# Kernel tuning notes

Measured on AMD Instinct MI355X. Metric: run time of the kernel, lower is better.

The kernel has to match this reference:

```python
import jax, jax.numpy as jnp
import numpy as np
import math

PHI = (1.0 + math.sqrt(5.0)) / 2.0
BASE_FAST = PHI
BASE_SLOW = 1618.0
D = 1024
NH = 16
HD = D // NH
H_GATE = max(8, D // 4)
B, L = 2, 2048


def _rope_cos_sin(seq_len, dim, base):
    # dim assumed even here (D=1024)
    idx = jnp.arange(0, dim, 2, dtype=jnp.float32) / float(dim)
    inv = 1.0 / (base ** idx)
    t = jnp.arange(seq_len, dtype=jnp.float32)
    freqs = jnp.outer(t, inv)                      # (L, dim/2)
    emb = jnp.concatenate([freqs, freqs], axis=-1) # (L, dim)
    return jnp.cos(emb), jnp.sin(emb)


def _rotate_half(x):
    d = x.shape[-1]
    x1, x2 = x[..., : d // 2], x[..., d // 2 :]
    return jnp.concatenate([-x2, x1], axis=-1)


def setup_inputs() -> dict:
    key = jax.random.key(0)
    ks = jax.random.split(key, 16)
    std = 0.02
    inp = {
        "z": jax.random.normal(ks[0], (B, L, D), jnp.float32),
        "pool_seq": jax.random.normal(ks[1], (B, L, D), jnp.float32),
        "Wq": std * jax.random.normal(ks[2], (D, D), jnp.float32),
        "bq": jnp.zeros((D,), jnp.float32),
        "Wk": std * jax.random.normal(ks[3], (D, D), jnp.float32),
        "bk": jnp.zeros((D,), jnp.float32),
        "Wv": std * jax.random.normal(ks[4], (D, D), jnp.float32),
        "bv": jnp.zeros((D,), jnp.float32),
        "W_coh": std * jax.random.normal(ks[5], (D, D), jnp.float32),
        "gamma": jnp.zeros((1,), jnp.float32) + 0.1,  # nonzero so bias path is exercised
        "Wg1": std * jax.random.normal(ks[6], (H_GATE, D), jnp.float32),
        "bg1": jnp.zeros((H_GATE,), jnp.float32),
        "Wg2": std * jax.random.normal(ks[7], (1, H_GATE), jnp.float32),
        "bg2": jnp.zeros((1,), jnp.float32),
    }
    return inp


def reference(z, pool_seq, Wq, bq, Wk, bk, Wv, bv, W_coh, gamma, Wg1, bg1, Wg2, bg2):
    b, l, d = z.shape
    # QKV projections (torch Linear: x @ W^T + b)
    Q = z @ Wq.T + bq
    K_raw = z @ Wk.T + bk
    V = z @ Wv.T + bv

    # Global coherence bias: per-query pool vector dotted with every key
    gk = pool_seq @ W_coh.T                                   # (B,L,D)
    gb = jnp.einsum("bqd,bkd->bqk", gk, K_raw) * (d ** -0.5)  # (B,L,L)
    gb = jnp.tanh(gamma[0]) * gb

    # Per-position RoPE interpolation gate (exact GELU as in torch default)
    h = jax.nn.gelu(pool_seq @ Wg1.T + bg1, approximate=False)
    gate = jax.nn.sigmoid(h @ Wg2.T + bg2)                    # (B,L,1)

    cos_f, sin_f = _rope_cos_sin(l, d, BASE_FAST)             # (L,D)
    cos_s, sin_s = _rope_cos_sin(l, d, BASE_SLOW)
    cos = gate * cos_f + (1.0 - gate) * cos_s                 # (B,L,D)
    sin = gate * sin_f + (1.0 - gate) * sin_s

    Q = Q * cos + _rotate_half(Q) * sin
    K_rot = K_raw * cos + _rotate_half(K_raw) * sin

    nh, hd = NH, d // NH
    Q_h = Q.reshape(b, l, nh, hd).transpose(0, 2, 1, 3)       # (B,H,L,hd)
    K_h = K_rot.reshape(b, l, nh, hd).transpose(0, 2, 1, 3)
    V_h = V.reshape(b, l, nh, hd).transpose(0, 2, 1, 3)

    logits = jnp.einsum("bhqd,bhkd->bhqk", Q_h, K_h) * (hd ** -0.5)
    logits = logits + gb[:, None]                             # broadcast over heads

    causal = jnp.tril(jnp.ones((l, l), dtype=bool))
    logits = jnp.where(causal[None, None], logits, -jnp.inf)

    attn_w_h = jax.nn.softmax(logits, axis=-1)                # (B,H,L,L)
    out_h = jnp.einsum("bhqk,bhkd->bhqd", attn_w_h, V_h)
    out = out_h.transpose(0, 2, 1, 3).reshape(b, l, d)
    attn_w = attn_w_h.mean(axis=1)                            # (B,L,L)
    return out, attn_w
```

## Files before the change

### kernel.cpp

```cpp
#include <hip/hip_runtime.h>
#include <hip/hip_bf16.h>

constexpr int Bn  = 2;
constexpr int Ln  = 2048;
constexpr int Dn  = 1024;
constexpr int NH  = 16;
constexpr int HGn = 256;
constexpr long BLD = (long)Bn * Ln * Dn;

typedef float f32x4 __attribute__((ext_vector_type(4)));
typedef float f32x2 __attribute__((ext_vector_type(2)));
typedef short s16x8 __attribute__((ext_vector_type(8)));
typedef short s16x4 __attribute__((ext_vector_type(4)));
typedef short s16x2 __attribute__((ext_vector_type(2)));

#define DEVI static __device__ __forceinline__

DEVI float bf2f(short u) {
  union { float f; unsigned int i; } v; v.i = ((unsigned int)(unsigned short)u) << 16; return v.f;
}
DEVI short f2bf(float f) {
  union { float f; unsigned int i; } v; v.f = f;
  unsigned int r = v.i + 0x7FFFu + ((v.i >> 16) & 1u);
  return (short)(r >> 16);
}
DEVI void gl_lds16(const void* g, void* l) {
  __builtin_amdgcn_global_load_lds((const __attribute__((address_space(1))) unsigned int*)g,
                                   (__attribute__((address_space(3))) unsigned int*)l, 16, 0, 0);
}

struct CastDesc { const float* src[7]; long cum[8]; };
__global__ void k_cast7(CastDesc d, short* __restrict__ dst) {
  long gi = ((long)blockIdx.x * 256 + threadIdx.x) * 4;
  int s = 0;
#pragma unroll
  for (int i = 1; i < 7; ++i) if (gi >= d.cum[i]) s = i;
  const float* sp = d.src[s] + (gi - d.cum[s]);
  f32x4 v = *(const f32x4*)sp;
  s16x4 o; o[0] = f2bf(v[0]); o[1] = f2bf(v[1]); o[2] = f2bf(v[2]); o[3] = f2bf(v[3]);
  *(s16x4*)(dst + gi) = o;
}

__global__ __launch_bounds__(512, 8)
void k_gemm_mega(const short* __restrict__ zb, const short* __restrict__ pb,
                 const short* __restrict__ Wcat,
                 const float* __restrict__ bq, const float* __restrict__ bk,
                 const float* __restrict__ bv, const float* __restrict__ bg1,
                 short* __restrict__ Qp, short* __restrict__ Kp,
                 short* __restrict__ Vtb, short* __restrict__ Gk,
                 short* __restrict__ Hfb) {
  int wgid = blockIdx.x;
  int xcd = wgid & 7, idx = wgid >> 3;
  int n0 = (idx >> 2) * 64;
  int m0 = (xcd * 4 + (idx & 3)) * 128;
  const short* Ap = (n0 < 3072) ? zb : pb;
  __shared__ short smA[2][128 * 32];
  __shared__ short smB[2][64 * 32];
  int tid = threadIdx.x;
  int lane = tid & 63, wid = tid >> 6;
  int wr = wid >> 1, wc = wid & 1;
  int lr = lane & 15, lg = lane >> 4;
  int r_in = lane >> 2;
  int slot = (lane & 3) * 8;
  int scol = ((lane & 3) ^ ((lane >> 3) & 3)) * 8;
  int rsw = (lr >> 1) & 3;
  f32x4 acc[2][2] = {};
  auto stage = [&](int buf, int k0) {
    int rowA = wid * 16 + r_in;
    gl_lds16(Ap + (long)(m0 + rowA) * Dn + k0 + scol, &smA[buf][rowA * 32 + slot]);
    if (wid < 4) {
      int rowB = wid * 16 + r_in;
      gl_lds16(Wcat + (long)(n0 + rowB) * Dn + k0 + scol, &smB[buf][rowB * 32 + slot]);
    }
  };
  stage(0, 0);
  int cur = 0;
  for (int k0 = 0; k0 < Dn; k0 += 32) {
    bool pre = (k0 + 32 < Dn);
    if (pre) stage(cur ^ 1, k0 + 32);
    __builtin_amdgcn_sched_barrier(0);
    if (pre) {
      if (wid < 4) asm volatile("s_waitcnt vmcnt(2)" ::: "memory");
      else         asm volatile("s_waitcnt vmcnt(1)" ::: "memory");
    } else {
      asm volatile("s_waitcnt vmcnt(0)" ::: "memory");
    }
    __builtin_amdgcn_s_barrier();
    __builtin_amdgcn_sched_barrier(0);
    const short* Ab = &smA[cur][(wr * 32 + lr) * 32 + ((lg ^ rsw) * 8)];
    const short* Bb = &smB[cur][(wc * 32 + lr) * 32 + ((lg ^ rsw) * 8)];
    s16x8 b0 = *(const s16x8*)(Bb);
    s16x8 b1 = *(const s16x8*)(Bb + 16 * 32);
    s16x8 a0 = *(const s16x8*)(Ab);
    s16x8 a1 = *(const s16x8*)(Ab + 16 * 32);
    acc[0][0] = __builtin_amdgcn_mfma_f32_16x16x32_bf16(a0, b0, acc[0][0], 0, 0, 0);
    acc[0][1] = __builtin_amdgcn_mfma_f32_16x16x32_bf16(a0, b1, acc[0][1], 0, 0, 0);
    acc[1][0] = __builtin_amdgcn_mfma_f32_16x16x32_bf16(a1, b0, acc[1][0], 0, 0, 0);
    acc[1][1] = __builtin_amdgcn_mfma_f32_16x16x32_bf16(a1, b1, acc[1][1], 0, 0, 0);
    __builtin_amdgcn_s_barrier();
    cur ^= 1;
  }
  int slice = n0 >> 10;
#pragma unroll
  for (int n = 0; n < 2; n++) {
    int col = n0 + wc * 32 + n * 16 + lr;
    int c = col - (slice << 10);
    float bias = (slice == 0) ? bq[c] : (slice == 1) ? bk[c] : (slice == 2) ? bv[c]
               : (slice == 3) ? 0.0f : bg1[c];
#pragma unroll
    for (int m = 0; m < 2; m++) {
#pragma unroll
      for (int r = 0; r < 4; r++) {
        long row = m0 + wr * 32 + m * 16 + lg * 4 + r;
        float v = acc[m][n][r] + bias;
        if (slice == 4) {
          v = 0.5f * v * (1.0f + erff(v * 0.70710678118f));
          Hfb[row * HGn + c] = f2bf(v);
        } else if (slice == 2) {
          long off = (((row >> 11) * (long)NH + (c >> 6)) * 64 + (c & 63)) * Ln + (row & (Ln - 1));
          Vtb[off] = f2bf(v);
        } else {
          short* dst = (slice == 0) ? Qp : (slice == 1) ? Kp : Gk;
          dst[row * (long)Dn + c] = f2bf(v);
        }
      }
    }
  }
}

__global__ __launch_bounds__(512, 8)
void k_gemm_gbd(const short* __restrict__ A, const short* __restrict__ B,
                const float* __restrict__ gamma, short* __restrict__ C) {
  int bz = blockIdx.y;
  int t0 = blockIdx.x;
  int qp = (int)((sqrtf(4.0f * (float)t0 + 1.0f) - 1.0f) * 0.5f);
  while ((qp + 1) * (qp + 2) <= t0) ++qp;
  while (qp * (qp + 1) > t0) --qp;
  int kp = t0 - qp * (qp + 1);
  int m0 = qp * 128, n0 = kp * 64;
  const short* Ap = A + (long)bz * Ln * Dn;
  const short* Bp = B + (long)bz * Ln * Dn;
  __shared__ short smA[2][128 * 32];
  __shared__ short smB[2][64 * 32];
  int tid = threadIdx.x;
  int lane = tid & 63, wid = tid >> 6;
  int wr = wid >> 1, wc = wid & 1;
  int lr = lane & 15, lg = lane >> 4;
  int r_in = lane >> 2;
  int slot = (lane & 3) * 8;
  int scol = ((lane & 3) ^ ((lane >> 3) & 3)) * 8;
  int rsw = (lr >> 1) & 3;
  f32x4 acc[2][2] = {};
  auto stage = [&](int buf, int k0) {
    int rowA = wid * 16 + r_in;
    gl_lds16(Ap + (long)(m0 + rowA) * Dn + k0 + scol, &smA[buf][rowA * 32 + slot]);
    if (wid < 4) {
      int rowB = wid * 16 + r_in;
      gl_lds16(Bp + (long)(n0 + rowB) * Dn + k0 + scol, &smB[buf][rowB * 32 + slot]);
    }
  };
  stage(0, 0);
  int cur = 0;
  for (int k0 = 0; k0 < Dn; k0 += 32) {
    bool pre = (k0 + 32 < Dn);
    if (pre) stage(cur ^ 1, k0 + 32);
    __builtin_amdgcn_sched_barrier(0);
    if (pre) {
      if (wid < 4) asm volatile("s_waitcnt vmcnt(2)" ::: "memory");
      else         asm volatile("s_waitcnt vmcnt(1)" ::: "memory");
    } else {
      asm volatile("s_waitcnt vmcnt(0)" ::: "memory");
    }
    __builtin_amdgcn_s_barrier();
    __builtin_amdgcn_sched_barrier(0);
    const short* Ab = &smA[cur][(wr * 32 + lr) * 32 + ((lg ^ rsw) * 8)];
    const short* Bb = &smB[cur][(wc * 32 + lr) * 32 + ((lg ^ rsw) * 8)];
    s16x8 b0 = *(const s16x8*)(Bb);
    s16x8 b1 = *(const s16x8*)(Bb + 16 * 32);
    s16x8 a0 = *(const s16x8*)(Ab);
    s16x8 a1 = *(const s16x8*)(Ab + 16 * 32);
    acc[0][0] = __builtin_amdgcn_mfma_f32_16x16x32_bf16(a0, b0, acc[0][0], 0, 0, 0);
    acc[0][1] = __builtin_amdgcn_mfma_f32_16x16x32_bf16(a0, b1, acc[0][1], 0, 0, 0);
    acc[1][0] = __builtin_amdgcn_mfma_f32_16x16x32_bf16(a1, b0, acc[1][0], 0, 0, 0);
    acc[1][1] = __builtin_amdgcn_mfma_f32_16x16x32_bf16(a1, b1, acc[1][1], 0, 0, 0);
    __builtin_amdgcn_s_barrier();
    cur ^= 1;
  }
  float alpha = tanhf(gamma[0]) * 0.03125f;
#pragma unroll
  for (int n = 0; n < 2; n++) {
    int col = n0 + wc * 32 + n * 16 + lr;
#pragma unroll
    for (int m = 0; m < 2; m++) {
#pragma unroll
      for (int r = 0; r < 4; r++) {
        long row = m0 + wr * 32 + m * 16 + lg * 4 + r;
        C[(long)bz * Ln * Ln + row * Ln + col] = f2bf(acc[m][n][r] * alpha);
      }
    }
  }
}

__global__ __launch_bounds__(256)
void k_rope_fused(short* __restrict__ Q, short* __restrict__ Kx,
                  const short* __restrict__ Hfb,
                  const float* __restrict__ Wg2, const float* __restrict__ bg2) {
  __shared__ float smG;
  int bl = blockIdx.x;
  int l = bl & (Ln - 1);
  int t = threadIdx.x;
  if (t < 64) {
    s16x4 h4 = *(const s16x4*)(Hfb + (long)bl * HGn + t * 4);
    f32x4 w = *(const f32x4*)(Wg2 + t * 4);
    float s = bf2f(h4[0]) * w[0] + bf2f(h4[1]) * w[1] + bf2f(h4[2]) * w[2] + bf2f(h4[3]) * w[3];
#pragma unroll
    for (int m = 1; m < 64; m <<= 1) s += __shfl_xor(s, m);
    if (t == 0) smG = 1.0f / (1.0f + __expf(-(s + bg2[0])));
  }
  __syncthreads();
  float g = smG;
  int j = t * 2;
  float e0 = (float)j * (1.0f / 512.0f);
  float e1 = (float)(j + 1) * (1.0f / 512.0f);
  float invf0 = powf(1.6180339887498949f, -e0);
  float invf1 = powf(1.6180339887498949f, -e1);
  float invs0 = powf(1618.0f, -e0);
  float invs1 = powf(1618.0f, -e1);
  float lf = (float)l;
  float sf0, cf0, sf1, cf1, ss0, cs0, ss1, cs1;
  sincosf(lf * invf0, &sf0, &cf0);
  sincosf(lf * invf1, &sf1, &cf1);
  sincosf(lf * invs0, &ss0, &cs0);
  sincosf(lf * invs1, &ss1, &cs1);
  float c0 = g * cf0 + (1.f - g) * cs0;
  float c1 = g * cf1 + (1.f - g) * cs1;
  float s0 = g * sf0 + (1.f - g) * ss0;
  float s1 = g * sf1 + (1.f - g) * ss1;
  long base = (long)bl * Dn + j;
  {
    s16x2 xa = *(const s16x2*)(Q + base);
    s16x2 xb = *(const s16x2*)(Q + base + 512);
    float a0 = bf2f(xa[0]), a1 = bf2f(xa[1]), b0 = bf2f(xb[0]), b1 = bf2f(xb[1]);
    s16x2 o0, o1;
    o0[0] = f2bf(a0 * c0 - b0 * s0); o0[1] = f2bf(a1 * c1 - b1 * s1);
    o1[0] = f2bf(b0 * c0 + a0 * s0); o1[1] = f2bf(b1 * c1 + a1 * s1);
    *(s16x2*)(Q + base) = o0;
    *(s16x2*)(Q + base + 512) = o1;
  }
  {
    s16x2 xa = *(const s16x2*)(Kx + base);
    s16x2 xb = *(const s16x2*)(Kx + base + 512);
    float a0 = bf2f(xa[0]), a1 = bf2f(xa[1]), b0 = bf2f(xb[0]), b1 = bf2f(xb[1]);
    s16x2 o0, o1;
    o0[0] = f2bf(a0 * c0 - b0 * s0); o0[1] = f2bf(a1 * c1 - b1 * s1);
    o1[0] = f2bf(b0 * c0 + a0 * s0); o1[1] = f2bf(b1 * c1 + a1 * s1);
    *(s16x2*)(Kx + base) = o0;
    *(s16x2*)(Kx + base + 512) = o1;
  }
}

__global__ __launch_bounds__(256)
void k_attn1(const short* __restrict__ Q, const short* __restrict__ Kx,
             const short* __restrict__ Vt, const short* __restrict__ Gb,
             float* __restrict__ outp, float* __restrict__ zinv) {
  int wg = blockIdx.x;
  int xcd = wg & 7, slot = wg >> 3;
  int p = slot & 15, gh = slot >> 4;
  int g = gh * 8 + xcd;
  int b = g >> 4, h = g & 15;

  int tid = threadIdx.x;
  int lane = tid & 63, w = tid >> 6;
  int lr = lane & 15, lg = lane >> 4;
  __shared__ short smK[2][64 * 64];
  __shared__ short smV[2][64 * 64];
  __shared__ short smP[4 * 16 * 64];
  short* pw = smP + w * 1024;

  int r0 = w * 16 + (lane >> 3);
  int scol = ((lane & 7) ^ (lane >> 3)) * 8;
  const short* Kg = Kx + (long)(b * Ln) * Dn + h * 64;
  const short* Vg = Vt + (long)(b * NH + h) * 64 * Ln;
  int sw = (lr & 7) << 3;

  for (int seg = 0; seg < 2; ++seg) {
    int qb = seg ? (31 - p) : p;
    int q0w = qb * 64 + w * 16;
    const short* qbp = Q + ((long)(b * Ln) + q0w + lr) * Dn + h * 64 + lg * 8;
    s16x8 qf0 = *(const s16x8*)(qbp);
    s16x8 qf1 = *(const s16x8*)(qbp + 32);
    f32x4 acc[4] = {};
    float az[4] = {0.f, 0.f, 0.f, 0.f};
    const short* gbase = Gb + ((long)b * Ln + q0w + lg * 4) * Ln + lr;

    int nt = qb + 1;
    auto stage = [&](int buf, int t) {
      long k0 = (long)t * 64;
      short* bK = &smK[buf][w * 1024];
      short* bV = &smV[buf][w * 1024];
      gl_lds16(Kg + (k0 + r0) * Dn + scol,           bK);
      gl_lds16(Kg + (k0 + r0 + 8) * Dn + scol,       bK + 512);
      gl_lds16(Vg + (long)r0 * Ln + k0 + scol,       bV);
      gl_lds16(Vg + (long)(r0 + 8) * Ln + k0 + scol, bV + 512);
    };

    float gcur[4][4], gnxt[4][4];
    stage(0, 0);
    {
      const short* g0 = gbase;
#pragma unroll
      for (int kk = 0; kk < 4; ++kk)
#pragma unroll
        for (int r = 0; r < 4; ++r) gcur[kk][r] = bf2f(g0[(long)r * Ln + kk * 16]);
    }
    int cur = 0;
    for (int t = 0; t < nt; ++t) {
      bool pre = (t + 1 < nt);
      if (pre) {
        const short* g0 = gbase + (t + 1) * 64;
#pragma unroll
        for (int kk = 0; kk < 4; ++kk)
#pragma unroll
          for (int r = 0; r < 4; ++r) gnxt[kk][r] = bf2f(g0[(long)r * Ln + kk * 16]);
        stage(cur ^ 1, t + 1);
      }
      __builtin_amdgcn_sched_barrier(0);
      if (pre) asm volatile("s_waitcnt vmcnt(20)" ::: "memory");
      else     asm volatile("s_waitcnt vmcnt(0)" ::: "memory");
      __builtin_amdgcn_s_barrier();
      __builtin_amdgcn_sched_barrier(0);
      int k0 = t * 64;
      const short* Kc = smK[cur];
      const short* Vc = smV[cur];
#pragma unroll
      for (int kk = 0; kk < 4; ++kk) {
        const short* kr = Kc + (kk * 16 + lr) * 64;
        s16x8 kf0 = *(const s16x8*)(kr + ((lg * 8) ^ sw));
        s16x8 kf1 = *(const s16x8*)(kr + ((32 + lg * 8) ^ sw));
        f32x4 S = {};
        S = __builtin_amdgcn_mfma_f32_16x16x32_bf16(qf0, kf0, S, 0, 0, 0);
        S = __builtin_amdgcn_mfma_f32_16x16x32_bf16(qf1, kf1, S, 0, 0, 0);
        int k = k0 + kk * 16 + lr;
#pragma unroll
        for (int r = 0; r < 4; r++) {
          int q = q0w + lg * 4 + r;
          float arg = (k <= q) ? (S[r] * 0.125f + gcur[kk][r]) : -80.0f;
          float pv = __expf(arg);
          az[r] += pv;
          int qq = lg * 4 + r;
          pw[qq * 64 + ((kk * 16 + lr) ^ ((qq & 7) << 3))] = f2bf(pv);
        }
      }
#pragma unroll
      for (int c = 0; c < 2; ++c) {
        s16x8 pf = *(const s16x8*)(pw + lr * 64 + ((c * 32 + lg * 8) ^ sw));
#pragma unroll
        for (int n = 0; n < 4; n++) {
          s16x8 vf = *(const s16x8*)(Vc + (n * 16 + lr) * 64 + ((c * 32 + lg * 8) ^ sw));
          acc[n] = __builtin_amdgcn_mfma_f32_16x16x32_bf16(pf, vf, acc[n], 0, 0, 0);
        }
      }
      __builtin_amdgcn_s_barrier();
      if (pre) {
#pragma unroll
        for (int kk = 0; kk < 4; ++kk)
#pragma unroll
          for (int r = 0; r < 4; ++r) gcur[kk][r] = gnxt[kk][r];
      }
      cur ^= 1;
    }
#pragma unroll
    for (int r = 0; r < 4; r++) {
      float z = az[r];
      z += __shfl_xor(z, 1); z += __shfl_xor(z, 2); z += __shfl_xor(z, 4); z += __shfl_xor(z, 8);
      az[r] = 1.0f / z;
    }
    if (lr == 0) {
#pragma unroll
      for (int r = 0; r < 4; r++)
        zinv[((long)(b * NH + h)) * Ln + q0w + lg * 4 + r] = az[r];
    }
#pragma unroll
    for (int n = 0; n < 4; n++) {
#pragma unroll
      for (int r = 0; r < 4; r++) {
        int q = q0w + lg * 4 + r;
        outp[((long)(b * Ln) + q) * Dn + h * 64 + n * 16 + lr] = acc[n][r] * az[r];
      }
    }
  }
}

__global__ __launch_bounds__(256)
void k_attn2(const short* __restrict__ Qm, const short* __restrict__ Kx,
             const short* __restrict__ Gb, const float* __restrict__ zinv, float* __restrict__ aw) {
  int b = blockIdx.y;
  int t = blockIdx.x;
  int qb = t >> 5, kb = t & 31;
  int q0 = qb * 64, k0 = kb * 64;
  int tid = threadIdx.x;
  if (kb > qb) {
    int row = tid >> 2, c4 = (tid & 3) << 4;
    float* basep = aw + ((long)b * Ln + q0 + row) * Ln + k0 + c4;
    f32x4 z = {};
    *(f32x4*)(basep) = z; *(f32x4*)(basep + 4) = z;
    *(f32x4*)(basep + 8) = z; *(f32x4*)(basep + 12) = z;
    return;
  }
  int lane = tid & 63, w = tid >> 6;
  int lr = lane & 15, lg = lane >> 4;
  int q0w = q0 + w * 16;
  bool diag = (qb == kb);
  __shared__ short smK[2][64 * 64];
  __shared__ short smQ[2][64 * 64];
  __shared__ float smZ[NH * 64];
  for (int i = tid; i < NH * 64; i += 256) {
    int h = i >> 6, qq = i & 63;
    smZ[i] = zinv[((long)(b * NH + h)) * Ln + q0 + qq];
  }
  __syncthreads();
  float gv[4][4];
#pragma unroll
  for (int n = 0; n < 4; n++) {
    int k = k0 + n * 16 + lr;
#pragma unroll
    for (int r = 0; r < 4; r++)
      gv[n][r] = bf2f(Gb[((long)b * Ln + q0w + lg * 4 + r) * Ln + k]);
  }
  int r0 = w * 16 + (lane >> 3);
  int scol = ((lane & 7) ^ (lane >> 3)) * 8;
  int sw = (lr & 7) << 3;
  auto stage = [&](int buf, int h) {
    short* bK = &smK[buf][w * 1024];
    short* bQ = &smQ[buf][w * 1024];
    const short* Kg = Kx + ((long)(b * Ln) + k0 + r0) * Dn + h * 64 + scol;
    gl_lds16(Kg, bK);
    gl_lds16(Kg + 8 * Dn, bK + 512);
    const short* Qg = Qm + ((long)(b * Ln) + q0 + r0) * Dn + h * 64 + scol;
    gl_lds16(Qg, bQ);
    gl_lds16(Qg + 8 * Dn, bQ + 512);
  };
  float wa[4][4] = {{0.f}};
  stage(0, 0);
  int cur = 0;
  for (int h = 0; h < NH; ++h) {
    bool pre = (h + 1 < NH);
    if (pre) stage(cur ^ 1, h + 1);
    __builtin_amdgcn_sched_barrier(0);
    if (pre) asm volatile("s_waitcnt vmcnt(4)" ::: "memory");
    else     asm volatile("s_waitcnt vmcnt(0)" ::: "memory");
    __builtin_amdgcn_s_barrier();
    __builtin_amdgcn_sched_barrier(0);
    const short* Kc = smK[cur];
    const short* Qc = smQ[cur];
    s16x8 qf0 = *(const s16x8*)(Qc + (w * 16 + lr) * 64 + ((lg * 8) ^ sw));
    s16x8 qf1 = *(const s16x8*)(Qc + (w * 16 + lr) * 64 + ((32 + lg * 8) ^ sw));
    float zq[4];
#pragma unroll
    for (int r = 0; r < 4; r++) zq[r] = smZ[h * 64 + w * 16 + lg * 4 + r];
#pragma unroll
    for (int n = 0; n < 4; n++) {
      const short* kr = Kc + (n * 16 + lr) * 64;
      s16x8 kf0 = *(const s16x8*)(kr + ((lg * 8) ^ sw));
      s16x8 kf1 = *(const s16x8*)(kr + ((32 + lg * 8) ^ sw));
      f32x4 S = {};
      S = __builtin_amdgcn_mfma_f32_16x16x32_bf16(qf0, kf0, S, 0, 0, 0);
      S = __builtin_amdgcn_mfma_f32_16x16x32_bf16(qf1, kf1, S, 0, 0, 0);
#pragma unroll
      for (int r = 0; r < 4; r++)
        wa[n][r] += __expf(S[r] * 0.125f + gv[n][r]) * zq[r];
    }
    __builtin_amdgcn_s_barrier();
    cur ^= 1;
  }
#pragma unroll
  for (int n = 0; n < 4; n++) {
    int k = k0 + n * 16 + lr;
#pragma unroll
    for (int r = 0; r < 4; r++) {
      int q = q0w + lg * 4 + r;
      float v = wa[n][r] * (1.0f / 16.0f);
      if (diag && k > q) v = 0.0f;
      aw[((long)b * Ln + q) * Ln + k] = v;
    }
  }
}

extern "C" void kernel_launch(void* const* d_in, const int* in_sizes, int n_in,
                              void* d_out, int out_size, void* d_ws, size_t ws_size,
                              hipStream_t stream) {
  const float* z    = (const float*)d_in[0];
  const float* ps   = (const float*)d_in[1];
  const float* Wq   = (const float*)d_in[2];
  const float* bq   = (const float*)d_in[3];
  const float* Wk   = (const float*)d_in[4];
  const float* bk   = (const float*)d_in[5];
  const float* Wv   = (const float*)d_in[6];
  const float* bv   = (const float*)d_in[7];
  const float* Wc   = (const float*)d_in[8];
  const float* gamma= (const float*)d_in[9];
  const float* Wg1  = (const float*)d_in[10];
  const float* bg1  = (const float*)d_in[11];
  const float* Wg2  = (const float*)d_in[12];
  const float* bg2  = (const float*)d_in[13];

  char* w = (char*)d_ws;
  auto alloc = [&](long bytes) { void* p = (void*)w; w += (bytes + 255) & ~255L; return p; };
  short* zb   = (short*)alloc(BLD * 2);
  short* pb   = (short*)alloc(BLD * 2);
  short* Wcat = (short*)alloc((long)(4 * Dn + HGn) * Dn * 2);
  short* Qp   = (short*)alloc(BLD * 2);
  short* Kp   = (short*)alloc(BLD * 2);
  short* Vtb  = (short*)alloc(BLD * 2);
  short* Gk   = (short*)alloc(BLD * 2);
  short* Hfb  = (short*)alloc((long)Bn * Ln * HGn * 2);
  float* zv   = (float*)alloc((long)Bn * NH * Ln * 4);
  short* Gb   = (short*)zb;

  float* outp = (float*)d_out;
  float* aw   = outp + BLD;

  CastDesc cd;
  cd.src[0] = z;  cd.src[1] = ps; cd.src[2] = Wq; cd.src[3] = Wk;
  cd.src[4] = Wv; cd.src[5] = Wc; cd.src[6] = Wg1;
  long c0 = 0;
  cd.cum[0] = 0;
  cd.cum[1] = (c0 += BLD);
  cd.cum[2] = (c0 += BLD);
  cd.cum[3] = (c0 += (long)Dn * Dn);
  cd.cum[4] = (c0 += (long)Dn * Dn);
  cd.cum[5] = (c0 += (long)Dn * Dn);
  cd.cum[6] = (c0 += (long)Dn * Dn);
  cd.cum[7] = (c0 += (long)HGn * Dn);
  k_cast7<<<(int)(c0 / 1024), 256, 0, stream>>>(cd, zb);

  k_gemm_mega<<<2176, 512, 0, stream>>>(zb, pb, Wcat, bq, bk, bv, bg1, Qp, Kp, Vtb, Gk, Hfb);

  k_gemm_gbd<<<dim3(272, Bn), 512, 0, stream>>>(Gk, Kp, gamma, Gb);

  k_rope_fused<<<Bn * Ln, 256, 0, stream>>>(Qp, Kp, Hfb, Wg2, bg2);

  k_attn1<<<512, 256, 0, stream>>>(Qp, Kp, Vtb, Gb, outp, zv);
  k_attn2<<<dim3(32 * 32, Bn), 256, 0, stream>>>(Qp, Kp, Gb, zv, aw);
}
```

Before: 227.0 us.

## Process two KV tiles per barrier step with paired double-buffered LDS staging

The causal attention loop now stages two 64-key K/V tiles per pipeline step, using a second LDS tile slot in each of the two buffers. Both tiles are computed between a single pair of barriers, and the bias values for both tiles are prefetched into registers. The aim is to halve the barrier and waitcnt overhead per key tile. In exchange, LDS use per block roughly doubles, which can lower occupancy. The new vmcnt thresholds (8/4) also look tighter than the number of loads issued, so the wait may stall on the prefetch that was just issued.

```diff
diff --git a/kernel.cpp b/kernel.cpp
--- a/kernel.cpp
+++ b/kernel.cpp
@@ -272,8 +272,8 @@
   int tid = threadIdx.x;
   int lane = tid & 63, w = tid >> 6;
   int lr = lane & 15, lg = lane >> 4;
-  __shared__ short smK[2][64 * 64];
-  __shared__ short smV[2][64 * 64];
+  __shared__ short smK[2][2][64 * 64];
+  __shared__ short smV[2][2][64 * 64];
   __shared__ short smP[4 * 16 * 64];
   short* pw = smP + w * 1024;
 
@@ -294,44 +294,26 @@
     const short* gbase = Gb + ((long)b * Ln + q0w + lg * 4) * Ln + lr;
 
     int nt = qb + 1;
-    auto stage = [&](int buf, int t) {
+    int ntc = (nt + 1) >> 1;
+
+    auto stageT = [&](int ps, int ti, int t) {
       long k0 = (long)t * 64;
-      short* bK = &smK[buf][w * 1024];
-      short* bV = &smV[buf][w * 1024];
+      short* bK = &smK[ps][ti][w * 1024];
+      short* bV = &smV[ps][ti][w * 1024];
       gl_lds16(Kg + (k0 + r0) * Dn + scol,           bK);
       gl_lds16(Kg + (k0 + r0 + 8) * Dn + scol,       bK + 512);
       gl_lds16(Vg + (long)r0 * Ln + k0 + scol,       bV);
       gl_lds16(Vg + (long)(r0 + 8) * Ln + k0 + scol, bV + 512);
     };
-
-    float gcur[4][4], gnxt[4][4];
-    stage(0, 0);
-    {
-      const short* g0 = gbase;
+    auto loadg = [&](float (&gd)[4][4], int t) {
+      const short* g0 = gbase + t * 64;
 #pragma unroll
       for (int kk = 0; kk < 4; ++kk)
 #pragma unroll
-        for (int r = 0; r < 4; ++r) gcur[kk][r] = bf2f(g0[(long)r * Ln + kk * 16]);
-    }
-    int cur = 0;
-    for (int t = 0; t < nt; ++t) {
-      bool pre = (t + 1 < nt);
-      if (pre) {
-        const short* g0 = gbase + (t + 1) * 64;
-#pragma unroll
-        for (int kk = 0; kk < 4; ++kk)
-#pragma unroll
-          for (int r = 0; r < 4; ++r) gnxt[kk][r] = bf2f(g0[(long)r * Ln + kk * 16]);
-        stage(cur ^ 1, t + 1);
-      }
-      __builtin_amdgcn_sched_barrier(0);
-      if (pre) asm volatile("s_waitcnt vmcnt(20)" ::: "memory");
-      else     asm volatile("s_waitcnt vmcnt(0)" ::: "memory");
-      __builtin_amdgcn_s_barrier();
-      __builtin_amdgcn_sched_barrier(0);
+        for (int r = 0; r < 4; ++r) gd[kk][r] = bf2f(g0[(long)r * Ln + kk * 16]);
+    };
+    auto compute = [&](const short* Kc, const short* Vc, float (&gc)[4][4], int t) {
       int k0 = t * 64;
-      const short* Kc = smK[cur];
-      const short* Vc = smV[cur];
 #pragma unroll
       for (int kk = 0; kk < 4; ++kk) {
         const short* kr = Kc + (kk * 16 + lr) * 64;
@@ -344,7 +326,7 @@
 #pragma unroll
         for (int r = 0; r < 4; r++) {
           int q = q0w + lg * 4 + r;
-          float arg = (k <= q) ? (S[r] * 0.125f + gcur[kk][r]) : -80.0f;
+          float arg = (k <= q) ? (S[r] * 0.125f + gc[kk][r]) : -80.0f;
           float pv = __expf(arg);
           az[r] += pv;
           int qq = lg * 4 + r;
@@ -360,12 +342,39 @@
           acc[n] = __builtin_amdgcn_mfma_f32_16x16x32_bf16(pf, vf, acc[n], 0, 0, 0);
         }
       }
+    };
+
+    float gc0[4][4], gc1[4][4], gn0[4][4], gn1[4][4];
+    stageT(0, 0, 0);
+    loadg(gc0, 0);
+    if (1 < nt) { stageT(0, 1, 1); loadg(gc1, 1); }
+    int cur = 0;
+    for (int tt = 0; tt < ntc; ++tt) {
+      int tB = 2 * tt + 1;
+      int tN0 = 2 * tt + 2, tN1 = 2 * tt + 3;
+      bool p0 = (tN0 < nt), p1 = (tN1 < nt);
+      if (p0) { loadg(gn0, tN0); stageT(cur ^ 1, 0, tN0); }
+      if (p1) { loadg(gn1, tN1); stageT(cur ^ 1, 1, tN1); }
+      __builtin_amdgcn_sched_barrier(0);
+      if (p1)      asm volatile("s_waitcnt vmcnt(8)" ::: "memory");
+      else if (p0) asm volatile("s_waitcnt vmcnt(4)" ::: "memory");
+      else         asm volatile("s_waitcnt vmcnt(0)" ::: "memory");
       __builtin_amdgcn_s_barrier();
-      if (pre) {
+      __builtin_amdgcn_sched_barrier(0);
+      compute(smK[cur][0], smV[cur][0], gc0, 2 * tt);
+      if (tB < nt) compute(smK[cur][1], smV[cur][1], gc1, tB);
+      __builtin_amdgcn_s_barrier();
+      if (p0) {
 #pragma unroll
         for (int kk = 0; kk < 4; ++kk)
 #pragma unroll
-          for (int r = 0; r < 4; ++r) gcur[kk][r] = gnxt[kk][r];
+          for (int r = 0; r < 4; ++r) gc0[kk][r] = gn0[kk][r];
+      }
+      if (p1) {
+#pragma unroll
+        for (int kk = 0; kk < 4; ++kk)
+#pragma unroll
+          for (int r = 0; r < 4; ++r) gc1[kk][r] = gn1[kk][r];
       }
       cur ^= 1;
     }
```

New measurement: 227.5 us. No clear change (+0.2%).
